# Performance work log

Measured on AMD Instinct MI355X. Metric: run time of the kernel, lower is better.

Reference implementation:

```python
import jax, jax.numpy as jnp
import numpy as np

N_NODES = 50000
N_EDGES = 800000
D_IN, H, D_OUT = 128, 128, 64


def setup_inputs() -> dict:
    key = jax.random.key(0)
    ks = jax.random.split(key, 8)
    x = jax.random.normal(ks[0], (N_NODES, D_IN), dtype=jnp.float32)
    edge_index = jax.random.randint(ks[1], (2, N_EDGES), 0, N_NODES, dtype=jnp.int64)
    s = 0.05
    return {
        "x": x,
        "edge_index": edge_index,
        # PyG Linear weights are [out, in]; y = x @ W.T + b
        "W_rel1": jax.random.normal(ks[2], (H, D_IN), dtype=jnp.float32) * s,
        "W_root1": jax.random.normal(ks[3], (H, D_IN), dtype=jnp.float32) * s,
        "b1": jax.random.normal(ks[4], (H,), dtype=jnp.float32) * s,
        "W_rel2": jax.random.normal(ks[5], (D_OUT, H), dtype=jnp.float32) * s,
        "W_root2": jax.random.normal(ks[6], (D_OUT, H), dtype=jnp.float32) * s,
        "b2": jax.random.normal(ks[7], (D_OUT,), dtype=jnp.float32) * s,
    }


def graph_conv(x, src, dst, W_rel, W_root, b):
    # sum-aggregate raw neighbor features, then apply linear (equivalent to
    # transforming each message first, but cheaper: one gather + one GEMM).
    agg = jax.ops.segment_sum(x[src], dst, num_segments=N_NODES)  # [N, D]
    return jnp.einsum('nd,hd->nh', agg, W_rel) \
         + jnp.einsum('nd,hd->nh', x, W_root) + b


def reference(x, edge_index, W_rel1, W_root1, b1, W_rel2, W_root2, b2):
    src, dst = edge_index[0], edge_index[1]  # messages flow src -> dst
    t = jax.nn.relu(graph_conv(x, src, dst, W_rel1, W_root1, b1))
    t = graph_conv(t, src, dst, W_rel2, W_root2, b2)
    return t
```

## Files before the change

### kernel.cpp

```cpp
#include <hip/hip_runtime.h>

#define NNODES 50000
#define DIM 128
#define SCAN_CHUNK 4096
#define NSCAN 13
#define PREP_BLOCKS 3200
#define POISON ((int)0xAAAAAAAA)

typedef __attribute__((ext_vector_type(8))) __bf16 bf16x8;
typedef __attribute__((ext_vector_type(4))) float f32x4;

__device__ inline unsigned short f2b(float f) {
    unsigned int u = __float_as_uint(f);
    u += 0x7fffu + ((u >> 16) & 1u);
    return (unsigned short)(u >> 16);
}
__device__ inline float blo(unsigned int u) { return __uint_as_float(u << 16); }
__device__ inline float bhi(unsigned int u) { return __uint_as_float(u & 0xffff0000u); }
__device__ inline unsigned int pack2(float a, float b) {
    return (unsigned int)f2b(a) | ((unsigned int)f2b(b) << 16);
}

__global__ __launch_bounds__(256) void k_prep(
    const float* __restrict__ x, unsigned short* __restrict__ xb, int n4,
    const float* __restrict__ Wa1, const float* __restrict__ Wb1,
    const float* __restrict__ Wa2, const float* __restrict__ Wb2,
    unsigned short* __restrict__ wa1, unsigned short* __restrict__ wb1,
    unsigned short* __restrict__ wa2, unsigned short* __restrict__ wb2,
    const int* __restrict__ dst, int* __restrict__ counts,
    unsigned short* __restrict__ rank, int n_edges)
{
    const int gid = blockIdx.x * 256 + threadIdx.x;

    const int i1 = blockIdx.x * 512 + threadIdx.x;
    const int i2 = i1 + 256;
    const bool ok1 = i1 < n4, ok2 = i2 < n4;
    float4 v1, v2;
    if (ok1) v1 = reinterpret_cast<const float4*>(x)[i1];
    if (ok2) v2 = reinterpret_cast<const float4*>(x)[i2];

    if (gid < n_edges)
        rank[gid] = (unsigned short)(atomicAdd(&counts[dst[gid]], 1) - POISON);

    if (gid < 16384) { wa1[gid] = f2b(Wa1[gid]); wb1[gid] = f2b(Wb1[gid]); }
    if (gid < 8192)  { wa2[gid] = f2b(Wa2[gid]); wb2[gid] = f2b(Wb2[gid]); }

    if (ok1) {
        uint2 o;
        o.x = pack2(v1.x, v1.y);
        o.y = pack2(v1.z, v1.w);
        reinterpret_cast<uint2*>(xb)[i1] = o;
    }
    if (ok2) {
        uint2 o;
        o.x = pack2(v2.x, v2.y);
        o.y = pack2(v2.z, v2.w);
        reinterpret_cast<uint2*>(xb)[i2] = o;
    }
}

__global__ __launch_bounds__(1024) void k_scan_local(
    const int* __restrict__ counts, int* __restrict__ rowptr,
    int* __restrict__ bsum, int n)
{
    __shared__ int wsum[16];
    const int lane = threadIdx.x & 63;
    const int wid = threadIdx.x >> 6;
    int i = blockIdx.x * SCAN_CHUNK + threadIdx.x * 4;
    int4 v = make_int4(0, 0, 0, 0);
    if (i + 3 < n) {
        v = *reinterpret_cast<const int4*>(counts + i);
        v.x -= POISON; v.y -= POISON; v.z -= POISON; v.w -= POISON;
    } else {
        if (i + 0 < n) v.x = counts[i + 0] - POISON;
        if (i + 1 < n) v.y = counts[i + 1] - POISON;
        if (i + 2 < n) v.z = counts[i + 2] - POISON;
    }
    int tot = v.x + v.y + v.z + v.w;
    int s = tot;
#pragma unroll
    for (int off = 1; off < 64; off <<= 1) {
        int t = __shfl_up(s, off);
        if (lane >= off) s += t;
    }
    if (lane == 63) wsum[wid] = s;
    __syncthreads();
    if (wid == 0 && lane < 16) {
        int ws = wsum[lane];
#pragma unroll
        for (int off = 1; off < 16; off <<= 1) {
            int t = __shfl_up(ws, off);
            if (lane >= off) ws += t;
        }
        wsum[lane] = ws;
    }
    __syncthreads();
    int prefix = ((wid > 0) ? wsum[wid - 1] : 0) + (s - tot);
    int4 o;
    o.x = prefix;
    o.y = prefix + v.x;
    o.z = o.y + v.y;
    o.w = o.z + v.z;
    if (i + 3 <= n) {
        *reinterpret_cast<int4*>(rowptr + i) = o;
    } else {
        if (i + 0 <= n) rowptr[i + 0] = o.x;
        if (i + 1 <= n) rowptr[i + 1] = o.y;
        if (i + 2 <= n) rowptr[i + 2] = o.z;
    }
    if (threadIdx.x == 1023) bsum[blockIdx.x] = wsum[15];
}

__device__ inline void build_prefix_lds(const int* __restrict__ bsum, int* pre) {
    if (threadIdx.x < 16) {
        int off = 0;
#pragma unroll 1
        for (int j = 0; j < NSCAN && j < (int)threadIdx.x; ++j) off += bsum[j];
        pre[threadIdx.x] = off;
    }
    __syncthreads();
}

__global__ __launch_bounds__(256) void k_place(
    const int* __restrict__ src, const int* __restrict__ dst,
    const unsigned short* __restrict__ rank, const int* __restrict__ rowptr,
    const int* __restrict__ bsum, unsigned short* __restrict__ srcs_sorted,
    int n_edges)
{
    __shared__ int pre[16];
    build_prefix_lds(bsum, pre);
    int e = (blockIdx.x * 256 + threadIdx.x) * 8;
    if (e + 7 < n_edges) {
        int4 s4a = *reinterpret_cast<const int4*>(src + e);
        int4 s4b = *reinterpret_cast<const int4*>(src + e + 4);
        int4 d4a = *reinterpret_cast<const int4*>(dst + e);
        int4 d4b = *reinterpret_cast<const int4*>(dst + e + 4);
        uint4 r8 = *reinterpret_cast<const uint4*>(rank + e);
        srcs_sorted[rowptr[d4a.x] + pre[d4a.x >> 12] + (int)(r8.x & 0xffffu)] = (unsigned short)s4a.x;
        srcs_sorted[rowptr[d4a.y] + pre[d4a.y >> 12] + (int)(r8.x >> 16)]     = (unsigned short)s4a.y;
        srcs_sorted[rowptr[d4a.z] + pre[d4a.z >> 12] + (int)(r8.y & 0xffffu)] = (unsigned short)s4a.z;
        srcs_sorted[rowptr[d4a.w] + pre[d4a.w >> 12] + (int)(r8.y >> 16)]     = (unsigned short)s4a.w;
        srcs_sorted[rowptr[d4b.x] + pre[d4b.x >> 12] + (int)(r8.z & 0xffffu)] = (unsigned short)s4b.x;
        srcs_sorted[rowptr[d4b.y] + pre[d4b.y >> 12] + (int)(r8.z >> 16)]     = (unsigned short)s4b.y;
        srcs_sorted[rowptr[d4b.z] + pre[d4b.z >> 12] + (int)(r8.w & 0xffffu)] = (unsigned short)s4b.z;
        srcs_sorted[rowptr[d4b.w] + pre[d4b.w >> 12] + (int)(r8.w >> 16)]     = (unsigned short)s4b.w;
    } else {
        for (; e < n_edges; ++e) {
            int d = dst[e];
            srcs_sorted[rowptr[d] + pre[d >> 12] + (int)rank[e]] = (unsigned short)src[e];
        }
    }
}

template <int BN>
__global__ __launch_bounds__(256) void k_gemm_dual(
    const unsigned short* __restrict__ A,
    const unsigned short* __restrict__ Wu,
    const unsigned short* __restrict__ Wr,
    const float* __restrict__ bias,
    unsigned short* __restrict__ U,
    unsigned short* __restrict__ R,
    int n_nodes)
{
    constexpr int NT = BN / 32;
    const int tid = threadIdx.x;
    const int wave = tid >> 6;
    const int lane = tid & 63;
    const int quad = lane >> 4;
    const int l16 = lane & 15;
    const int wr = wave >> 1;
    const int wc = wave & 1;
    const int rl = wr * 16 + l16;
    const int n0 = blockIdx.x * 32;
    const int arow = n0 + rl;
    const bool ok = arow < n_nodes;

    f32x4 accU[NT], accR[NT];
#pragma unroll
    for (int nt = 0; nt < NT; ++nt) {
        f32x4 z = {0.f, 0.f, 0.f, 0.f};
        accU[nt] = z;
        accR[nt] = z;
    }

#pragma unroll 1
    for (int kk = 0; kk < 2; ++kk) {
        const int ko = kk * 64;
        bf16x8 a0 = {}, a1 = {};
        if (ok) {
            a0 = *reinterpret_cast<const bf16x8*>(A + (size_t)arow * DIM + ko + quad * 8);
            a1 = *reinterpret_cast<const bf16x8*>(A + (size_t)arow * DIM + ko + 32 + quad * 8);
        }
#pragma unroll
        for (int nt = 0; nt < NT; ++nt) {
            const size_t woff = (size_t)(wc * (BN / 2) + nt * 16 + l16) * DIM + ko + quad * 8;
            bf16x8 bu0 = *reinterpret_cast<const bf16x8*>(Wu + woff);
            bf16x8 br0 = *reinterpret_cast<const bf16x8*>(Wr + woff);
            accU[nt] = __builtin_amdgcn_mfma_f32_16x16x32_bf16(a0, bu0, accU[nt], 0, 0, 0);
            accR[nt] = __builtin_amdgcn_mfma_f32_16x16x32_bf16(a0, br0, accR[nt], 0, 0, 0);
            bf16x8 bu1 = *reinterpret_cast<const bf16x8*>(Wu + woff + 32);
            bf16x8 br1 = *reinterpret_cast<const bf16x8*>(Wr + woff + 32);
            accU[nt] = __builtin_amdgcn_mfma_f32_16x16x32_bf16(a1, bu1, accU[nt], 0, 0, 0);
            accR[nt] = __builtin_amdgcn_mfma_f32_16x16x32_bf16(a1, br1, accR[nt], 0, 0, 0);
        }
    }

#pragma unroll
    for (int nt = 0; nt < NT; ++nt) {
        const int col = wc * (BN / 2) + nt * 16 + l16;
        const float bv = bias[col];
#pragma unroll
        for (int reg = 0; reg < 4; ++reg) {
            const int row = n0 + wr * 16 + quad * 4 + reg;
            if (row >= n_nodes) continue;
            U[(size_t)row * BN + col] = f2b(accU[nt][reg]);
            R[(size_t)row * BN + col] = f2b(accR[nt][reg] + bv);
        }
    }
}

__global__ __launch_bounds__(256) void k_gather_ep1(
    const unsigned short* __restrict__ U, const unsigned short* __restrict__ R,
    const int* __restrict__ rowptr, const int* __restrict__ bsum,
    const unsigned short* __restrict__ srcs, unsigned short* __restrict__ T)
{
    __shared__ int pre[16];
    build_prefix_lds(bsum, pre);
    int node = blockIdx.x * 16 + (threadIdx.x >> 4);
    if (node >= NNODES) return;
    int seg = threadIdx.x & 15;
    int beg = rowptr[node] + pre[node >> 12];
    int end = rowptr[node + 1] + pre[(node + 1) >> 12];
    float acc[8];
#pragma unroll
    for (int i = 0; i < 8; ++i) acc[i] = 0.f;
    int e = beg;
#pragma unroll 1
    for (; e + 7 < end; e += 8) {
        uint4 v[8];
#pragma unroll
        for (int u = 0; u < 8; ++u) {
            int s = srcs[e + u];
            v[u] = *reinterpret_cast<const uint4*>(U + (size_t)s * DIM + seg * 8);
        }
#pragma unroll
        for (int u = 0; u < 8; ++u) {
            acc[0] += blo(v[u].x); acc[1] += bhi(v[u].x);
            acc[2] += blo(v[u].y); acc[3] += bhi(v[u].y);
            acc[4] += blo(v[u].z); acc[5] += bhi(v[u].z);
            acc[6] += blo(v[u].w); acc[7] += bhi(v[u].w);
        }
    }
#pragma unroll 1
    for (; e + 1 < end; e += 2) {
        int s0 = srcs[e], s1 = srcs[e + 1];
        uint4 v0 = *reinterpret_cast<const uint4*>(U + (size_t)s0 * DIM + seg * 8);
        uint4 v1 = *reinterpret_cast<const uint4*>(U + (size_t)s1 * DIM + seg * 8);
        acc[0] += blo(v0.x) + blo(v1.x); acc[1] += bhi(v0.x) + bhi(v1.x);
        acc[2] += blo(v0.y) + blo(v1.y); acc[3] += bhi(v0.y) + bhi(v1.y);
        acc[4] += blo(v0.z) + blo(v1.z); acc[5] += bhi(v0.z) + bhi(v1.z);
        acc[6] += blo(v0.w) + blo(v1.w); acc[7] += bhi(v0.w) + bhi(v1.w);
    }
    if (e < end) {
        int s0 = srcs[e];
        uint4 v = *reinterpret_cast<const uint4*>(U + (size_t)s0 * DIM + seg * 8);
        acc[0] += blo(v.x); acc[1] += bhi(v.x);
        acc[2] += blo(v.y); acc[3] += bhi(v.y);
        acc[4] += blo(v.z); acc[5] += bhi(v.z);
        acc[6] += blo(v.w); acc[7] += bhi(v.w);
    }
    uint4 rv = *reinterpret_cast<const uint4*>(R + (size_t)node * DIM + seg * 8);
    acc[0] += blo(rv.x); acc[1] += bhi(rv.x);
    acc[2] += blo(rv.y); acc[3] += bhi(rv.y);
    acc[4] += blo(rv.z); acc[5] += bhi(rv.z);
    acc[6] += blo(rv.w); acc[7] += bhi(rv.w);
#pragma unroll
    for (int i = 0; i < 8; ++i) acc[i] = fmaxf(acc[i], 0.f);
    uint4 o;
    o.x = pack2(acc[0], acc[1]);
    o.y = pack2(acc[2], acc[3]);
    o.z = pack2(acc[4], acc[5]);
    o.w = pack2(acc[6], acc[7]);
    *reinterpret_cast<uint4*>(T + (size_t)node * DIM + seg * 8) = o;
}

__global__ __launch_bounds__(256) void k_gather_ep2(
    const unsigned short* __restrict__ U, const unsigned short* __restrict__ R,
    const int* __restrict__ rowptr, const int* __restrict__ bsum,
    const unsigned short* __restrict__ srcs, float* __restrict__ out)
{
    __shared__ int pre[16];
    build_prefix_lds(bsum, pre);
    int node = blockIdx.x * 32 + (threadIdx.x >> 3);
    if (node >= NNODES) return;
    int seg = threadIdx.x & 7;
    int beg = rowptr[node] + pre[node >> 12];
    int end = rowptr[node + 1] + pre[(node + 1) >> 12];
    float acc[8];
#pragma unroll
    for (int i = 0; i < 8; ++i) acc[i] = 0.f;
    int e = beg;
#pragma unroll 1
    for (; e + 7 < end; e += 8) {
        uint4 v[8];
#pragma unroll
        for (int u = 0; u < 8; ++u) {
            int s = srcs[e + u];
            v[u] = *reinterpret_cast<const uint4*>(U + (size_t)s * 64 + seg * 8);
        }
#pragma unroll
        for (int u = 0; u < 8; ++u) {
            acc[0] += blo(v[u].x); acc[1] += bhi(v[u].x);
            acc[2] += blo(v[u].y); acc[3] += bhi(v[u].y);
            acc[4] += blo(v[u].z); acc[5] += bhi(v[u].z);
            acc[6] += blo(v[u].w); acc[7] += bhi(v[u].w);
        }
    }
#pragma unroll 1
    for (; e + 1 < end; e += 2) {
        int s0 = srcs[e], s1 = srcs[e + 1];
        uint4 v0 = *reinterpret_cast<const uint4*>(U + (size_t)s0 * 64 + seg * 8);
        uint4 v1 = *reinterpret_cast<const uint4*>(U + (size_t)s1 * 64 + seg * 8);
        acc[0] += blo(v0.x) + blo(v1.x); acc[1] += bhi(v0.x) + bhi(v1.x);
        acc[2] += blo(v0.y) + blo(v1.y); acc[3] += bhi(v0.y) + bhi(v1.y);
        acc[4] += blo(v0.z) + blo(v1.z); acc[5] += bhi(v0.z) + bhi(v1.z);
        acc[6] += blo(v0.w) + blo(v1.w); acc[7] += bhi(v0.w) + bhi(v1.w);
    }
    if (e < end) {
        int s0 = srcs[e];
        uint4 v = *reinterpret_cast<const uint4*>(U + (size_t)s0 * 64 + seg * 8);
        acc[0] += blo(v.x); acc[1] += bhi(v.x);
        acc[2] += blo(v.y); acc[3] += bhi(v.y);
        acc[4] += blo(v.z); acc[5] += bhi(v.z);
        acc[6] += blo(v.w); acc[7] += bhi(v.w);
    }
    uint4 rv = *reinterpret_cast<const uint4*>(R + (size_t)node * 64 + seg * 8);
    acc[0] += blo(rv.x); acc[1] += bhi(rv.x);
    acc[2] += blo(rv.y); acc[3] += bhi(rv.y);
    acc[4] += blo(rv.z); acc[5] += bhi(rv.z);
    acc[6] += blo(rv.w); acc[7] += bhi(rv.w);
    float4 o0 = make_float4(acc[0], acc[1], acc[2], acc[3]);
    float4 o1 = make_float4(acc[4], acc[5], acc[6], acc[7]);
    float* op = out + (size_t)node * 64 + seg * 8;
    *reinterpret_cast<float4*>(op) = o0;
    *reinterpret_cast<float4*>(op + 4) = o1;
}

extern "C" void kernel_launch(void* const* d_in, const int* in_sizes, int n_in,
                              void* d_out, int out_size, void* d_ws, size_t ws_size,
                              hipStream_t stream) {
    const float* x       = (const float*)d_in[0];
    const int*   ei      = (const int*)d_in[1];
    const float* W_rel1  = (const float*)d_in[2];
    const float* W_root1 = (const float*)d_in[3];
    const float* b1      = (const float*)d_in[4];
    const float* W_rel2  = (const float*)d_in[5];
    const float* W_root2 = (const float*)d_in[6];
    const float* b2      = (const float*)d_in[7];

    const int n_edges = in_sizes[1] / 2;
    const int* src = ei;
    const int* dst = ei + n_edges;

    const size_t NELEM = (size_t)NNODES * DIM;
    unsigned short* xb   = (unsigned short*)d_ws;
    unsigned short* tb   = xb + NELEM;
    unsigned short* u1   = tb + NELEM;
    unsigned short* r1   = u1 + NELEM;
    unsigned short* u2   = r1 + NELEM;
    unsigned short* r2   = u2 + (size_t)NNODES * 64;
    unsigned short* wa1  = r2 + (size_t)NNODES * 64;
    unsigned short* wb1  = wa1 + 16384;
    unsigned short* wa2  = wb1 + 16384;
    unsigned short* wb2  = wa2 + 8192;
    int* counts = (int*)(wb2 + 8192);
    int* rowptr = counts + NNODES;
    int* bsum   = rowptr + (NNODES + 4);
    unsigned short* rank16 = (unsigned short*)(bsum + 20);
    unsigned short* srcs16 = rank16 + n_edges;

    float* out = (float*)d_out;

    const int n4 = NNODES * DIM / 4;
    const int pblocks = (n_edges + 2047) / 2048;
    const int g1blocks = (NNODES + 15) / 16;
    const int g2blocks = (NNODES + 31) / 32;
    const int gemm_blocks = (NNODES + 31) / 32;
    const int sblocks = NSCAN;

    k_prep<<<PREP_BLOCKS, 256, 0, stream>>>(
        x, xb, n4, W_rel1, W_root1, W_rel2, W_root2,
        wa1, wb1, wa2, wb2, dst, counts, rank16, n_edges);

    k_gemm_dual<128><<<gemm_blocks, 256, 0, stream>>>(
        xb, wa1, wb1, b1, u1, r1, NNODES);

    k_scan_local<<<sblocks, 1024, 0, stream>>>(counts, rowptr, bsum, NNODES);
    k_place<<<pblocks, 256, 0, stream>>>(src, dst, rank16, rowptr, bsum, srcs16, n_edges);

    k_gather_ep1<<<g1blocks, 256, 0, stream>>>(u1, r1, rowptr, bsum, srcs16, tb);

    k_gemm_dual<64><<<gemm_blocks, 256, 0, stream>>>(
        tb, wa2, wb2, b2, u2, r2, NNODES);
    k_gather_ep2<<<g2blocks, 256, 0, stream>>>(u2, r2, rowptr, bsum, srcs16, out);
}
```

Baseline: 245.8 us.

## Replicate per-node edge counters four ways and vectorize GEMM output stores

Edge counting now spreads atomics over four replicated counter arrays chosen by lane, which is meant to cut atomic contention on hot destination nodes. The scan merges the replicas and stores per-replica offsets, and placement uses them to compute slots. Separately, the GEMM swaps its MFMA operand order so each lane holds four consecutive columns of one row, allowing packed 8-byte stores and a float4 bias load. The launch order is also changed so the CSR build runs before the first GEMM. Costs are an extra per-node offset read in placement and four times the counter memory, and the rank field now has only 14 bits.

```diff
diff --git a/kernel.cpp b/kernel.cpp
--- a/kernel.cpp
+++ b/kernel.cpp
@@ -39,8 +39,11 @@
     if (ok1) v1 = reinterpret_cast<const float4*>(x)[i1];
     if (ok2) v2 = reinterpret_cast<const float4*>(x)[i2];
 
-    if (gid < n_edges)
-        rank[gid] = (unsigned short)(atomicAdd(&counts[dst[gid]], 1) - POISON);
+    if (gid < n_edges) {
+        const int rep = threadIdx.x & 3;
+        int rk = atomicAdd(&counts[rep * NNODES + dst[gid]], 1) - POISON;
+        rank[gid] = (unsigned short)(rk | (rep << 14));
+    }
 
     if (gid < 16384) { wa1[gid] = f2b(Wa1[gid]); wb1[gid] = f2b(Wb1[gid]); }
     if (gid < 8192)  { wa2[gid] = f2b(Wa2[gid]); wb2[gid] = f2b(Wb2[gid]); }
@@ -61,7 +64,7 @@
 
 __global__ __launch_bounds__(1024) void k_scan_local(
     const int* __restrict__ counts, int* __restrict__ rowptr,
-    int* __restrict__ bsum, int n)
+    int* __restrict__ bsum, uint2* __restrict__ repx2, int n)
 {
     __shared__ int wsum[16];
     const int lane = threadIdx.x & 63;
@@ -69,12 +72,47 @@
     int i = blockIdx.x * SCAN_CHUNK + threadIdx.x * 4;
     int4 v = make_int4(0, 0, 0, 0);
     if (i + 3 < n) {
-        v = *reinterpret_cast<const int4*>(counts + i);
-        v.x -= POISON; v.y -= POISON; v.z -= POISON; v.w -= POISON;
+        int4 c0 = *reinterpret_cast<const int4*>(counts + i);
+        int4 c1 = *reinterpret_cast<const int4*>(counts + NNODES + i);
+        int4 c2 = *reinterpret_cast<const int4*>(counts + 2 * NNODES + i);
+        int4 c3 = *reinterpret_cast<const int4*>(counts + 3 * NNODES + i);
+        c0.x -= POISON; c0.y -= POISON; c0.z -= POISON; c0.w -= POISON;
+        c1.x -= POISON; c1.y -= POISON; c1.z -= POISON; c1.w -= POISON;
+        c2.x -= POISON; c2.y -= POISON; c2.z -= POISON; c2.w -= POISON;
+        c3.x -= POISON; c3.y -= POISON; c3.z -= POISON; c3.w -= POISON;
+        v.x = c0.x + c1.x + c2.x + c3.x;
+        v.y = c0.y + c1.y + c2.y + c3.y;
+        v.z = c0.z + c1.z + c2.z + c3.z;
+        v.w = c0.w + c1.w + c2.w + c3.w;
+        uint2 r0, r1g, r2g, r3g;
+        r0.x  = (unsigned)(c0.x) << 16;
+        r0.y  = (unsigned)(c0.x + c1.x) | ((unsigned)(c0.x + c1.x + c2.x) << 16);
+        r1g.x = (unsigned)(c0.y) << 16;
+        r1g.y = (unsigned)(c0.y + c1.y) | ((unsigned)(c0.y + c1.y + c2.y) << 16);
+        r2g.x = (unsigned)(c0.z) << 16;
+        r2g.y = (unsigned)(c0.z + c1.z) | ((unsigned)(c0.z + c1.z + c2.z) << 16);
+        r3g.x = (unsigned)(c0.w) << 16;
+        r3g.y = (unsigned)(c0.w + c1.w) | ((unsigned)(c0.w + c1.w + c2.w) << 16);
+        repx2[i + 0] = r0;
+        repx2[i + 1] = r1g;
+        repx2[i + 2] = r2g;
+        repx2[i + 3] = r3g;
     } else {
-        if (i + 0 < n) v.x = counts[i + 0] - POISON;
-        if (i + 1 < n) v.y = counts[i + 1] - POISON;
-        if (i + 2 < n) v.z = counts[i + 2] - POISON;
+#pragma unroll
+        for (int j = 0; j < 3; ++j) {
+            if (i + j < n) {
+                int c0 = counts[i + j] - POISON;
+                int c1 = counts[NNODES + i + j] - POISON;
+                int c2 = counts[2 * NNODES + i + j] - POISON;
+                int c3 = counts[3 * NNODES + i + j] - POISON;
+                int t = c0 + c1 + c2 + c3;
+                if (j == 0) v.x = t; else if (j == 1) v.y = t; else v.z = t;
+                uint2 r;
+                r.x = (unsigned)c0 << 16;
+                r.y = (unsigned)(c0 + c1) | ((unsigned)(c0 + c1 + c2) << 16);
+                repx2[i + j] = r;
+            }
+        }
     }
     int tot = v.x + v.y + v.z + v.w;
     int s = tot;
@@ -121,11 +159,16 @@
     __syncthreads();
 }
 
+__device__ inline int rep_off(uint2 rp, int r) {
+    unsigned pw = (r & 2) ? rp.y : rp.x;
+    return (r & 1) ? (int)(pw >> 16) : (int)(pw & 0xffffu);
+}
+
 __global__ __launch_bounds__(256) void k_place(
     const int* __restrict__ src, const int* __restrict__ dst,
     const unsigned short* __restrict__ rank, const int* __restrict__ rowptr,
-    const int* __restrict__ bsum, unsigned short* __restrict__ srcs_sorted,
-    int n_edges)
+    const int* __restrict__ bsum, const uint2* __restrict__ repx2,
+    unsigned short* __restrict__ srcs_sorted, int n_edges)
 {
     __shared__ int pre[16];
     build_prefix_lds(bsum, pre);
@@ -136,18 +179,31 @@
         int4 d4a = *reinterpret_cast<const int4*>(dst + e);
         int4 d4b = *reinterpret_cast<const int4*>(dst + e + 4);
         uint4 r8 = *reinterpret_cast<const uint4*>(rank + e);
-        srcs_sorted[rowptr[d4a.x] + pre[d4a.x >> 12] + (int)(r8.x & 0xffffu)] = (unsigned short)s4a.x;
-        srcs_sorted[rowptr[d4a.y] + pre[d4a.y >> 12] + (int)(r8.x >> 16)]     = (unsigned short)s4a.y;
-        srcs_sorted[rowptr[d4a.z] + pre[d4a.z >> 12] + (int)(r8.y & 0xffffu)] = (unsigned short)s4a.z;
-        srcs_sorted[rowptr[d4a.w] + pre[d4a.w >> 12] + (int)(r8.y >> 16)]     = (unsigned short)s4a.w;
-        srcs_sorted[rowptr[d4b.x] + pre[d4b.x >> 12] + (int)(r8.z & 0xffffu)] = (unsigned short)s4b.x;
-        srcs_sorted[rowptr[d4b.y] + pre[d4b.y >> 12] + (int)(r8.z >> 16)]     = (unsigned short)s4b.y;
-        srcs_sorted[rowptr[d4b.z] + pre[d4b.z >> 12] + (int)(r8.w & 0xffffu)] = (unsigned short)s4b.z;
-        srcs_sorted[rowptr[d4b.w] + pre[d4b.w >> 12] + (int)(r8.w >> 16)]     = (unsigned short)s4b.w;
+        unsigned rk[8];
+        rk[0] = r8.x & 0xffffu; rk[1] = r8.x >> 16;
+        rk[2] = r8.y & 0xffffu; rk[3] = r8.y >> 16;
+        rk[4] = r8.z & 0xffffu; rk[5] = r8.z >> 16;
+        rk[6] = r8.w & 0xffffu; rk[7] = r8.w >> 16;
+        int dd[8] = {d4a.x, d4a.y, d4a.z, d4a.w, d4b.x, d4b.y, d4b.z, d4b.w};
+        int ss[8] = {s4a.x, s4a.y, s4a.z, s4a.w, s4b.x, s4b.y, s4b.z, s4b.w};
+#pragma unroll
+        for (int j = 0; j < 8; ++j) {
+            const int d = dd[j];
+            const int r = (int)(rk[j] >> 14);
+            const int rv = (int)(rk[j] & 0x3fffu);
+            uint2 rp = repx2[d];
+            srcs_sorted[rowptr[d] + pre[d >> 12] + rep_off(rp, r) + rv] =
+                (unsigned short)ss[j];
+        }
     } else {
         for (; e < n_edges; ++e) {
             int d = dst[e];
-            srcs_sorted[rowptr[d] + pre[d >> 12] + (int)rank[e]] = (unsigned short)src[e];
+            unsigned rk16 = rank[e];
+            int r = (int)(rk16 >> 14);
+            int rv = (int)(rk16 & 0x3fffu);
+            uint2 rp = repx2[d];
+            srcs_sorted[rowptr[d] + pre[d >> 12] + rep_off(rp, r) + rv] =
+                (unsigned short)src[e];
         }
     }
 }
@@ -170,10 +226,9 @@
     const int l16 = lane & 15;
     const int wr = wave >> 1;
     const int wc = wave & 1;
-    const int rl = wr * 16 + l16;
     const int n0 = blockIdx.x * 32;
-    const int arow = n0 + rl;
-    const bool ok = arow < n_nodes;
+    const int node = n0 + wr * 16 + l16;
+    const bool ok = node < n_nodes;
 
     f32x4 accU[NT], accR[NT];
 #pragma unroll
@@ -188,33 +243,35 @@
         const int ko = kk * 64;
         bf16x8 a0 = {}, a1 = {};
         if (ok) {
-            a0 = *reinterpret_cast<const bf16x8*>(A + (size_t)arow * DIM + ko + quad * 8);
-            a1 = *reinterpret_cast<const bf16x8*>(A + (size_t)arow * DIM + ko + 32 + quad * 8);
+            a0 = *reinterpret_cast<const bf16x8*>(A + (size_t)node * DIM + ko + quad * 8);
+            a1 = *reinterpret_cast<const bf16x8*>(A + (size_t)node * DIM + ko + 32 + quad * 8);
         }
 #pragma unroll
         for (int nt = 0; nt < NT; ++nt) {
             const size_t woff = (size_t)(wc * (BN / 2) + nt * 16 + l16) * DIM + ko + quad * 8;
             bf16x8 bu0 = *reinterpret_cast<const bf16x8*>(Wu + woff);
             bf16x8 br0 = *reinterpret_cast<const bf16x8*>(Wr + woff);
-            accU[nt] = __builtin_amdgcn_mfma_f32_16x16x32_bf16(a0, bu0, accU[nt], 0, 0, 0);
-            accR[nt] = __builtin_amdgcn_mfma_f32_16x16x32_bf16(a0, br0, accR[nt], 0, 0, 0);
+            accU[nt] = __builtin_amdgcn_mfma_f32_16x16x32_bf16(bu0, a0, accU[nt], 0, 0, 0);
+            accR[nt] = __builtin_amdgcn_mfma_f32_16x16x32_bf16(br0, a0, accR[nt], 0, 0, 0);
             bf16x8 bu1 = *reinterpret_cast<const bf16x8*>(Wu + woff + 32);
             bf16x8 br1 = *reinterpret_cast<const bf16x8*>(Wr + woff + 32);
-            accU[nt] = __builtin_amdgcn_mfma_f32_16x16x32_bf16(a1, bu1, accU[nt], 0, 0, 0);
-            accR[nt] = __builtin_amdgcn_mfma_f32_16x16x32_bf16(a1, br1, accR[nt], 0, 0, 0);
-        }
-    }
-
-#pragma unroll
-    for (int nt = 0; nt < NT; ++nt) {
-        const int col = wc * (BN / 2) + nt * 16 + l16;
-        const float bv = bias[col];
-#pragma unroll
-        for (int reg = 0; reg < 4; ++reg) {
-            const int row = n0 + wr * 16 + quad * 4 + reg;
-            if (row >= n_nodes) continue;
-            U[(size_t)row * BN + col] = f2b(accU[nt][reg]);
-            R[(size_t)row * BN + col] = f2b(accR[nt][reg] + bv);
+            accU[nt] = __builtin_amdgcn_mfma_f32_16x16x32_bf16(bu1, a1, accU[nt], 0, 0, 0);
+            accR[nt] = __builtin_amdgcn_mfma_f32_16x16x32_bf16(br1, a1, accR[nt], 0, 0, 0);
+        }
+    }
+
+    if (ok) {
+#pragma unroll
+        for (int nt = 0; nt < NT; ++nt) {
+            const int colb = wc * (BN / 2) + nt * 16 + quad * 4;
+            const float4 bv = *reinterpret_cast<const float4*>(bias + colb);
+            uint2 uo, ro;
+            uo.x = pack2(accU[nt][0], accU[nt][1]);
+            uo.y = pack2(accU[nt][2], accU[nt][3]);
+            ro.x = pack2(accR[nt][0] + bv.x, accR[nt][1] + bv.y);
+            ro.y = pack2(accR[nt][2] + bv.z, accR[nt][3] + bv.w);
+            *reinterpret_cast<uint2*>(U + (size_t)node * BN + colb) = uo;
+            *reinterpret_cast<uint2*>(R + (size_t)node * BN + colb) = ro;
         }
     }
 }
@@ -374,9 +431,10 @@
     unsigned short* wa2  = wb1 + 16384;
     unsigned short* wb2  = wa2 + 8192;
     int* counts = (int*)(wb2 + 8192);
-    int* rowptr = counts + NNODES;
+    int* rowptr = counts + 4 * NNODES;
     int* bsum   = rowptr + (NNODES + 4);
-    unsigned short* rank16 = (unsigned short*)(bsum + 20);
+    uint2* repx2 = (uint2*)(bsum + 20);
+    unsigned short* rank16 = (unsigned short*)(repx2 + NNODES);
     unsigned short* srcs16 = rank16 + n_edges;
 
     float* out = (float*)d_out;
@@ -392,11 +450,12 @@
         x, xb, n4, W_rel1, W_root1, W_rel2, W_root2,
         wa1, wb1, wa2, wb2, dst, counts, rank16, n_edges);
 
+    k_scan_local<<<sblocks, 1024, 0, stream>>>(counts, rowptr, bsum, repx2, NNODES);
+    k_place<<<pblocks, 256, 0, stream>>>(src, dst, rank16, rowptr, bsum, repx2,
+                                         srcs16, n_edges);
+
     k_gemm_dual<128><<<gemm_blocks, 256, 0, stream>>>(
         xb, wa1, wb1, b1, u1, r1, NNODES);
-
-    k_scan_local<<<sblocks, 1024, 0, stream>>>(counts, rowptr, bsum, NNODES);
-    k_place<<<pblocks, 256, 0, stream>>>(src, dst, rank16, rowptr, bsum, srcs16, n_edges);
 
     k_gather_ep1<<<g1blocks, 256, 0, stream>>>(u1, r1, rowptr, bsum, srcs16, tb);
 
```

New measurement: 245.0 us. About the same (-0.3%).
